# Optimization experiments

Measured on AMD Instinct MI355X. Metric: run time of the kernel, lower is better.

Reference implementation:

```python
import jax, jax.numpy as jnp
import numpy as np

N_ATOMS = 100000
N_FEAT = 256
N_MOL = 1024
SCALE = 5.992277830325989
SHIFT = -406274.63784969115


def setup_inputs() -> dict:
    key = jax.random.key(0)
    ks = jax.random.split(key, 8)
    atom_node = jax.random.normal(ks[0], (N_ATOMS, N_FEAT), dtype=jnp.float32)
    batch = jnp.sort(jax.random.randint(ks[1], (N_ATOMS,), 0, N_MOL, dtype=jnp.int64))
    s = 1.0 / np.sqrt(N_FEAT)
    W1 = jax.random.normal(ks[2], (N_FEAT, N_FEAT), dtype=jnp.float32) * s
    b1 = jnp.zeros((N_FEAT,), dtype=jnp.float32)
    W2 = jax.random.normal(ks[3], (N_FEAT, N_FEAT), dtype=jnp.float32) * s
    b2 = jnp.zeros((N_FEAT,), dtype=jnp.float32)
    W3 = jax.random.normal(ks[4], (N_FEAT, 1), dtype=jnp.float32) * s
    b3 = jnp.zeros((1,), dtype=jnp.float32)
    return {"atom_node": atom_node, "batch": batch, "W1": W1, "b1": b1,
            "W2": W2, "b2": b2, "W3": W3, "b3": b3}


def reference(atom_node, batch, W1, b1, W2, b2, W3, b3):
    # atom-wise 3-layer MLP: F -> F -> F -> 1 with SiLU activations
    h = jax.nn.silu(atom_node @ W1 + b1)          # [N, F]
    h = jax.nn.silu(h @ W2 + b2)                  # [N, F]
    e_atom = (h @ W3 + b3)[:, 0]                  # [N]
    # scatter-sum pooling over molecules
    e_mol = jax.ops.segment_sum(e_atom, batch, num_segments=N_MOL)  # [N_MOL]
    # affine rescale (hardcoded scaler constants from the module)
    return e_mol * SCALE + SHIFT
```

## Files before the change

### kernel.cpp

```cpp
#include <hip/hip_runtime.h>
#include <hip/hip_bf16.h>
#include <cstdint>

#define N_ATOMS 100000
#define NFEAT   256
#define NMOL    1024
#define NU      6256

static constexpr float SCALE_C = 5.992277830325989f;
static constexpr float SHIFT_C = -406274.63784969115f;

typedef __attribute__((ext_vector_type(8))) short short8;
typedef __attribute__((ext_vector_type(4))) float float4_t;

__device__ __forceinline__ unsigned short f2bf(float x) {
    union { float f; uint32_t u; } v; v.f = x;
    uint32_t r = (v.u + 0x7fffu + ((v.u >> 16) & 1u)) >> 16;
    return (unsigned short)r;
}

__device__ __forceinline__ uint32_t pk(float lo, float hi) {
    union { float f; uint32_t u; } a, b; a.f = lo; b.f = hi;
    return __builtin_amdgcn_perm(b.u + 0x8000u, a.u + 0x8000u, 0x07060302u);
}

__device__ __forceinline__ float silu(float x) {
    return x / (1.0f + __expf(-x));
}

__device__ __forceinline__ void async16(void* lds, const void* g) {
    __builtin_amdgcn_global_load_lds(
        (const __attribute__((address_space(1))) unsigned int*)(uintptr_t)g,
        (__attribute__((address_space(3))) unsigned int*)(uint32_t)(uintptr_t)lds,
        16, 0, 0);
}

__device__ __forceinline__ short8 wfrag(const unsigned short* Wlds, int n, int kc) {
    return *(const short8*)&Wlds[((kc >> 4) << 15) + n * 128 +
                                 ((((kc & 15) ^ (n & 15)) & 15) << 3)];
}

__global__ void prep(const float* __restrict__ W1, const float* __restrict__ W2,
                     unsigned short* __restrict__ W1i, unsigned short* __restrict__ W2i,
                     float* __restrict__ out) {
    int g = blockIdx.x * 256 + threadIdx.x;
    const float* W = (g < 65536) ? W1 : W2;
    unsigned short* Wi = (g < 65536) ? W1i : W2i;
    int idx = g & 65535;
    int k = idx >> 8, n = idx & 255;
    int kc = (k >> 3) & 15;
    int pos = ((k >> 7) << 15) + n * 128 + (((kc ^ (n & 15)) & 15) << 3) + (k & 7);
    Wi[pos] = f2bf(W[idx]);
    if (g < NMOL) out[g] = SHIFT_C;
}

__global__ __launch_bounds__(512, 2)
void gemm1(const float* __restrict__ A, const unsigned short* __restrict__ Wimg,
           const float* __restrict__ b1, unsigned short* __restrict__ H1) {
    __shared__ unsigned short Wlds[65536];
    __shared__ float b1L[256];
    __shared__ int uctr;

    const int tid = threadIdx.x;
    const int w = tid >> 6, lane = tid & 63;
    const int fl = lane & 15, qd = lane >> 4;

#pragma unroll
    for (int i = 0; i < 16; ++i)
        async16(&Wlds[(w * 16 + i) * 512], Wimg + (w * 16 + i) * 512 + lane * 8);
    if (tid < 64) ((float4*)b1L)[tid] = ((const float4*)b1)[tid];
    if (tid == 0) uctr = 0;
    __syncthreads();

    for (;;) {
        int t = 0;
        if (lane == 0) t = atomicAdd(&uctr, 1);
        t = __shfl(t, 0);
        const int u = blockIdx.x + (t << 8);
        if (u >= NU) break;

        const int row = u * 16 + fl;
        const bool valid = row < N_ATOMS;
        const float* ap = A + (size_t)row * 256 + qd * 8;

        float4 c0, c1;
        if (valid) { c0 = *(const float4*)ap; c1 = *(const float4*)(ap + 4); }
        else       { c0 = make_float4(0, 0, 0, 0); c1 = c0; }

        float4_t acc[16] = {};
#pragma unroll
        for (int s = 0; s < 8; ++s) {
            float4 n0 = make_float4(0, 0, 0, 0), n1 = n0;
            if (s < 7 && valid) {
                n0 = *(const float4*)(ap + (s + 1) * 32);
                n1 = *(const float4*)(ap + (s + 1) * 32 + 4);
            }
            union { uint32_t u4[4]; short8 s8; } cv;
            cv.u4[0] = pk(c0.x, c0.y); cv.u4[1] = pk(c0.z, c0.w);
            cv.u4[2] = pk(c1.x, c1.y); cv.u4[3] = pk(c1.z, c1.w);
            const int kc = s * 4 + qd;
#pragma unroll
            for (int j = 0; j < 16; ++j) {
                short8 wf = wfrag(Wlds, j * 16 + fl, kc);
                acc[j] = __builtin_amdgcn_mfma_f32_16x16x32_bf16(wf, cv.s8, acc[j], 0, 0, 0);
            }
            c0 = n0; c1 = n1;
        }

        if (valid) {
#pragma unroll
            for (int j = 0; j < 16; ++j) {
                int nb = j * 16 + qd * 4;
                float4 b4 = *(const float4*)&b1L[nb];
                uint2 o;
                o.x = pk(silu(acc[j][0] + b4.x), silu(acc[j][1] + b4.y));
                o.y = pk(silu(acc[j][2] + b4.z), silu(acc[j][3] + b4.w));
                *(uint2*)&H1[(size_t)row * 256 + nb] = o;
            }
        }
    }
}

__global__ __launch_bounds__(512, 2)
void gemm2(const unsigned short* __restrict__ H1, const unsigned short* __restrict__ Wimg,
           const float* __restrict__ b2, const float* __restrict__ W3,
           const float* __restrict__ b3, const int* __restrict__ batch,
           float* __restrict__ out) {
    __shared__ unsigned short Wlds[65536];
    __shared__ float bucket[NMOL];
    __shared__ int uctr;

    const int tid = threadIdx.x;
    const int w = tid >> 6, lane = tid & 63;
    const int fl = lane & 15, qd = lane >> 4;

#pragma unroll
    for (int i = 0; i < 16; ++i)
        async16(&Wlds[(w * 16 + i) * 512], Wimg + (w * 16 + i) * 512 + lane * 8);
    bucket[tid] = 0.0f;
    bucket[tid + 512] = 0.0f;
    if (tid == 0) uctr = 0;
    __syncthreads();

    const float b3v = b3[0];
    float bbv[16], w3v[16];
#pragma unroll
    for (int nt = 0; nt < 16; ++nt) {
        bbv[nt] = b2[nt * 16 + fl];
        w3v[nt] = W3[nt * 16 + fl];
    }

    for (;;) {
        int t = 0;
        if (lane == 0) t = atomicAdd(&uctr, 1);
        t = __shfl(t, 0);
        const int u = blockIdx.x + (t << 8);
        if (u >= NU) break;

        const int ubase = u * 16;
        const int row = ubase + fl;
        const bool valid = row < N_ATOMS;
        const unsigned short* hp = H1 + (size_t)row * 256 + qd * 8;

        short8 h0 = (short8){0, 0, 0, 0, 0, 0, 0, 0};
        if (valid) h0 = *(const short8*)hp;

        float4_t acc[16] = {};
#pragma unroll
        for (int s = 0; s < 8; ++s) {
            short8 hn = (short8){0, 0, 0, 0, 0, 0, 0, 0};
            if (s < 7 && valid) hn = *(const short8*)(hp + (s + 1) * 32);
            const int kc = s * 4 + qd;
#pragma unroll
            for (int nt = 0; nt < 16; ++nt) {
                short8 wf = wfrag(Wlds, nt * 16 + fl, kc);
                acc[nt] = __builtin_amdgcn_mfma_f32_16x16x32_bf16(h0, wf, acc[nt], 0, 0, 0);
            }
            h0 = hn;
        }

        float rs[4] = {};
#pragma unroll
        for (int nt = 0; nt < 16; ++nt)
#pragma unroll
            for (int r = 0; r < 4; ++r)
                rs[r] += silu(acc[nt][r] + bbv[nt]) * w3v[nt];
#pragma unroll
        for (int r = 0; r < 4; ++r) {
            float v = rs[r];
            v += __shfl_xor(v, 1);
            v += __shfl_xor(v, 2);
            v += __shfl_xor(v, 4);
            v += __shfl_xor(v, 8);
            rs[r] = v;
        }
        if (fl == 0) {
            int atom0 = ubase + qd * 4;
            if (atom0 < N_ATOMS) {
                int4 mb = *(const int4*)&batch[atom0];
                float v0 = rs[0] + b3v, v1 = rs[1] + b3v,
                      v2 = rs[2] + b3v, v3 = rs[3] + b3v;
                if (mb.x == mb.w) {
                    atomicAdd(&bucket[mb.x], (v0 + v1) + (v2 + v3));
                } else {
                    atomicAdd(&bucket[mb.x], v0);
                    atomicAdd(&bucket[mb.y], v1);
                    atomicAdd(&bucket[mb.z], v2);
                    atomicAdd(&bucket[mb.w], v3);
                }
            }
        }
    }
    __syncthreads();
#pragma unroll
    for (int i = 0; i < 2; ++i) {
        int m = tid + i * 512;
        float v = bucket[m];
        if (v != 0.0f) atomicAdd(&out[m], v * SCALE_C);
    }
}

extern "C" void kernel_launch(void* const* d_in, const int* in_sizes, int n_in,
                              void* d_out, int out_size, void* d_ws, size_t ws_size,
                              hipStream_t stream) {
    const float* A     = (const float*)d_in[0];
    const int*   batch = (const int*)d_in[1];
    const float* W1    = (const float*)d_in[2];
    const float* b1    = (const float*)d_in[3];
    const float* W2    = (const float*)d_in[4];
    const float* b2    = (const float*)d_in[5];
    const float* W3    = (const float*)d_in[6];
    const float* b3    = (const float*)d_in[7];
    float* out = (float*)d_out;

    unsigned short* H1  = (unsigned short*)d_ws;
    unsigned short* W1i = H1 + (size_t)100096 * NFEAT;
    unsigned short* W2i = W1i + 65536;

    prep<<<dim3(512), 256, 0, stream>>>(W1, W2, W1i, W2i, out);
    gemm1<<<dim3(256), 512, 0, stream>>>(A, W1i, b1, H1);
    gemm2<<<dim3(256), 512, 0, stream>>>(H1, W2i, b2, W3, b3, batch, out);
}
```

Measured before the change: 208.5 us.

## Split output features across two block groups to halve LDS weight footprint

Each GEMM kernel now launches twice as many blocks. Each block loads only half of the weight matrix (128 output columns) into LDS and computes that half of the outputs. LDS per block is halved, so more blocks can be resident per CU (launch bounds raised to 4), which should improve latency hiding. In exchange, every block group re-reads the full input rows (A in fp32 for gemm1, H1 for gemm2), roughly doubling global input traffic, and gemm2 issues twice the bucket atomics.

```diff
diff --git a/kernel.cpp b/kernel.cpp
--- a/kernel.cpp
+++ b/kernel.cpp
@@ -35,9 +35,9 @@
         16, 0, 0);
 }
 
-__device__ __forceinline__ short8 wfrag(const unsigned short* Wlds, int n, int kc) {
-    return *(const short8*)&Wlds[((kc >> 4) << 15) + n * 128 +
-                                 ((((kc & 15) ^ (n & 15)) & 15) << 3)];
+__device__ __forceinline__ short8 wfrag_h(const unsigned short* Wlds, int nl, int kc) {
+    return *(const short8*)&Wlds[((kc >> 4) << 14) + nl * 128 +
+                                 ((((kc & 15) ^ (nl & 15)) & 15) << 3)];
 }
 
 __global__ void prep(const float* __restrict__ W1, const float* __restrict__ W2,
@@ -54,21 +54,26 @@
     if (g < NMOL) out[g] = SHIFT_C;
 }
 
-__global__ __launch_bounds__(512, 2)
+__global__ __launch_bounds__(512, 4)
 void gemm1(const float* __restrict__ A, const unsigned short* __restrict__ Wimg,
            const float* __restrict__ b1, unsigned short* __restrict__ H1) {
-    __shared__ unsigned short Wlds[65536];
-    __shared__ float b1L[256];
+    __shared__ unsigned short Wlds[32768];
+    __shared__ float b1L[128];
     __shared__ int uctr;
 
     const int tid = threadIdx.x;
     const int w = tid >> 6, lane = tid & 63;
     const int fl = lane & 15, qd = lane >> 4;
-
-#pragma unroll
-    for (int i = 0; i < 16; ++i)
-        async16(&Wlds[(w * 16 + i) * 512], Wimg + (w * 16 + i) * 512 + lane * 8);
-    if (tid < 64) ((float4*)b1L)[tid] = ((const float4*)b1)[tid];
+    const int ch = blockIdx.x >> 8;
+    const int bslot = blockIdx.x & 255;
+
+#pragma unroll
+    for (int i = 0; i < 8; ++i) {
+        int c = w * 8 + i;
+        async16(&Wlds[c * 512],
+                Wimg + ((c >> 5) << 15) + (ch << 14) + ((c & 31) << 9) + lane * 8);
+    }
+    if (tid < 32) ((float4*)b1L)[tid] = ((const float4*)(b1 + ch * 128))[tid];
     if (tid == 0) uctr = 0;
     __syncthreads();
 
@@ -76,7 +81,7 @@
         int t = 0;
         if (lane == 0) t = atomicAdd(&uctr, 1);
         t = __shfl(t, 0);
-        const int u = blockIdx.x + (t << 8);
+        const int u = bslot + (t << 8);
         if (u >= NU) break;
 
         const int row = u * 16 + fl;
@@ -87,7 +92,7 @@
         if (valid) { c0 = *(const float4*)ap; c1 = *(const float4*)(ap + 4); }
         else       { c0 = make_float4(0, 0, 0, 0); c1 = c0; }
 
-        float4_t acc[16] = {};
+        float4_t acc[8] = {};
 #pragma unroll
         for (int s = 0; s < 8; ++s) {
             float4 n0 = make_float4(0, 0, 0, 0), n1 = n0;
@@ -100,8 +105,8 @@
             cv.u4[2] = pk(c1.x, c1.y); cv.u4[3] = pk(c1.z, c1.w);
             const int kc = s * 4 + qd;
 #pragma unroll
-            for (int j = 0; j < 16; ++j) {
-                short8 wf = wfrag(Wlds, j * 16 + fl, kc);
+            for (int j = 0; j < 8; ++j) {
+                short8 wf = wfrag_h(Wlds, j * 16 + fl, kc);
                 acc[j] = __builtin_amdgcn_mfma_f32_16x16x32_bf16(wf, cv.s8, acc[j], 0, 0, 0);
             }
             c0 = n0; c1 = n1;
@@ -109,52 +114,57 @@
 
         if (valid) {
 #pragma unroll
-            for (int j = 0; j < 16; ++j) {
-                int nb = j * 16 + qd * 4;
-                float4 b4 = *(const float4*)&b1L[nb];
+            for (int j = 0; j < 8; ++j) {
+                int nl = j * 16 + qd * 4;
+                float4 b4 = *(const float4*)&b1L[nl];
                 uint2 o;
                 o.x = pk(silu(acc[j][0] + b4.x), silu(acc[j][1] + b4.y));
                 o.y = pk(silu(acc[j][2] + b4.z), silu(acc[j][3] + b4.w));
-                *(uint2*)&H1[(size_t)row * 256 + nb] = o;
-            }
-        }
-    }
-}
-
-__global__ __launch_bounds__(512, 2)
+                *(uint2*)&H1[(size_t)row * 256 + ch * 128 + nl] = o;
+            }
+        }
+    }
+}
+
+__global__ __launch_bounds__(512, 4)
 void gemm2(const unsigned short* __restrict__ H1, const unsigned short* __restrict__ Wimg,
            const float* __restrict__ b2, const float* __restrict__ W3,
            const float* __restrict__ b3, const int* __restrict__ batch,
            float* __restrict__ out) {
-    __shared__ unsigned short Wlds[65536];
+    __shared__ unsigned short Wlds[32768];
     __shared__ float bucket[NMOL];
     __shared__ int uctr;
 
     const int tid = threadIdx.x;
     const int w = tid >> 6, lane = tid & 63;
     const int fl = lane & 15, qd = lane >> 4;
-
-#pragma unroll
-    for (int i = 0; i < 16; ++i)
-        async16(&Wlds[(w * 16 + i) * 512], Wimg + (w * 16 + i) * 512 + lane * 8);
+    const int ch = blockIdx.x >> 8;
+    const int bslot = blockIdx.x & 255;
+
+#pragma unroll
+    for (int i = 0; i < 8; ++i) {
+        int c = w * 8 + i;
+        async16(&Wlds[c * 512],
+                Wimg + ((c >> 5) << 15) + (ch << 14) + ((c & 31) << 9) + lane * 8);
+    }
     bucket[tid] = 0.0f;
     bucket[tid + 512] = 0.0f;
     if (tid == 0) uctr = 0;
     __syncthreads();
 
-    const float b3v = b3[0];
-    float bbv[16], w3v[16];
-#pragma unroll
-    for (int nt = 0; nt < 16; ++nt) {
-        bbv[nt] = b2[nt * 16 + fl];
-        w3v[nt] = W3[nt * 16 + fl];
+    const float b3v = (ch == 0) ? b3[0] : 0.0f;
+    float bbv[8], w3v[8];
+#pragma unroll
+    for (int nt = 0; nt < 8; ++nt) {
+        bbv[nt] = b2[ch * 128 + nt * 16 + fl];
+        w3v[nt] = W3[ch * 128 + nt * 16 + fl];
     }
 
     for (;;) {
         int t = 0;
         if (lane == 0) t = atomicAdd(&uctr, 1);
         t = __shfl(t, 0);
-        const int u = blockIdx.x + (t << 8);
+        const int u = bslot + (t << 8);
         if (u >= NU) break;
 
         const int ubase = u * 16;
@@ -165,15 +175,15 @@
         short8 h0 = (short8){0, 0, 0, 0, 0, 0, 0, 0};
         if (valid) h0 = *(const short8*)hp;
 
-        float4_t acc[16] = {};
+        float4_t acc[8] = {};
 #pragma unroll
         for (int s = 0; s < 8; ++s) {
             short8 hn = (short8){0, 0, 0, 0, 0, 0, 0, 0};
             if (s < 7 && valid) hn = *(const short8*)(hp + (s + 1) * 32);
             const int kc = s * 4 + qd;
 #pragma unroll
-            for (int nt = 0; nt < 16; ++nt) {
-                short8 wf = wfrag(Wlds, nt * 16 + fl, kc);
+            for (int nt = 0; nt < 8; ++nt) {
+                short8 wf = wfrag_h(Wlds, nt * 16 + fl, kc);
                 acc[nt] = __builtin_amdgcn_mfma_f32_16x16x32_bf16(h0, wf, acc[nt], 0, 0, 0);
             }
             h0 = hn;
@@ -181,7 +191,7 @@
 
         float rs[4] = {};
 #pragma unroll
-        for (int nt = 0; nt < 16; ++nt)
+        for (int nt = 0; nt < 8; ++nt)
 #pragma unroll
             for (int r = 0; r < 4; ++r)
                 rs[r] += silu(acc[nt][r] + bbv[nt]) * w3v[nt];
@@ -238,6 +248,6 @@
     unsigned short* W2i = W1i + 65536;
 
     prep<<<dim3(512), 256, 0, stream>>>(W1, W2, W1i, W2i, out);
-    gemm1<<<dim3(256), 512, 0, stream>>>(A, W1i, b1, H1);
-    gemm2<<<dim3(256), 512, 0, stream>>>(H1, W2i, b2, W3, b3, batch, out);
-}
+    gemm1<<<dim3(512), 512, 0, stream>>>(A, W1i, b1, H1);
+    gemm2<<<dim3(512), 512, 0, stream>>>(H1, W2i, b2, W3, b3, batch, out);
+}
```

Measured after the change: 210.8 us. Within noise of the previous version (+1.1%).

## Pre-convert activations to bf16 in prep and prefetch full row tiles

Applied to the files above, without the earlier changes.

The prep kernel now also converts the fp32 atom features to a padded bf16 buffer, zero-filling the pad rows. gemm1 therefore reads half the bytes per tile and no longer needs row-validity checks. Both GEMMs load all eight K-slices of a row tile up front and fetch the next work index early, and gemm2 moves b2/W3 from registers into LDS. The extra pass over A adds a full read plus a bf16 write before gemm1, and the up-front loads raise register pressure.

```diff
diff --git a/kernel.cpp b/kernel.cpp
--- a/kernel.cpp
+++ b/kernel.cpp
@@ -6,6 +6,7 @@
 #define NFEAT   256
 #define NMOL    1024
 #define NU      6256
+#define NPAD    100096
 
 static constexpr float SCALE_C = 5.992277830325989f;
 static constexpr float SHIFT_C = -406274.63784969115f;
@@ -41,21 +42,40 @@
 }
 
 __global__ void prep(const float* __restrict__ W1, const float* __restrict__ W2,
+                     const float* __restrict__ A,
                      unsigned short* __restrict__ W1i, unsigned short* __restrict__ W2i,
-                     float* __restrict__ out) {
-    int g = blockIdx.x * 256 + threadIdx.x;
-    const float* W = (g < 65536) ? W1 : W2;
-    unsigned short* Wi = (g < 65536) ? W1i : W2i;
-    int idx = g & 65535;
-    int k = idx >> 8, n = idx & 255;
-    int kc = (k >> 3) & 15;
-    int pos = ((k >> 7) << 15) + n * 128 + (((kc ^ (n & 15)) & 15) << 3) + (k & 7);
-    Wi[pos] = f2bf(W[idx]);
-    if (g < NMOL) out[g] = SHIFT_C;
+                     unsigned short* __restrict__ Ab, float* __restrict__ out) {
+    const int b = blockIdx.x, tid = threadIdx.x;
+    if (b < 512) {
+        int g = b * 256 + tid;
+        const float* W = (g < 65536) ? W1 : W2;
+        unsigned short* Wi = (g < 65536) ? W1i : W2i;
+        int idx = g & 65535;
+        int k = idx >> 8, n = idx & 255;
+        int kc = (k >> 3) & 15;
+        int pos = ((k >> 7) << 15) + n * 128 + (((kc ^ (n & 15)) & 15) << 3) + (k & 7);
+        Wi[pos] = f2bf(W[idx]);
+        if (g < NMOL) out[g] = SHIFT_C;
+    } else if (b < 6762) {
+        int t = (b - 512) * 256 + tid;
+        const float4* af = (const float4*)(A + (size_t)t * 16);
+        float4 x0 = af[0], x1 = af[1], x2 = af[2], x3 = af[3];
+        uint4 o0 = make_uint4(pk(x0.x, x0.y), pk(x0.z, x0.w),
+                              pk(x1.x, x1.y), pk(x1.z, x1.w));
+        uint4 o1 = make_uint4(pk(x2.x, x2.y), pk(x2.z, x2.w),
+                              pk(x3.x, x3.y), pk(x3.z, x3.w));
+        ((uint4*)Ab)[(size_t)t * 2]     = o0;
+        ((uint4*)Ab)[(size_t)t * 2 + 1] = o1;
+    } else {
+        int idx = (b - 6762) * 256 + tid;
+        uint4 z = make_uint4(0, 0, 0, 0);
+        ((uint4*)(Ab + (size_t)N_ATOMS * 256))[idx * 2]     = z;
+        ((uint4*)(Ab + (size_t)N_ATOMS * 256))[idx * 2 + 1] = z;
+    }
 }
 
 __global__ __launch_bounds__(512, 2)
-void gemm1(const float* __restrict__ A, const unsigned short* __restrict__ Wimg,
+void gemm1(const unsigned short* __restrict__ Ab, const unsigned short* __restrict__ Wimg,
            const float* __restrict__ b1, unsigned short* __restrict__ H1) {
     __shared__ unsigned short Wlds[65536];
     __shared__ float b1L[256];
@@ -64,6 +84,7 @@
     const int tid = threadIdx.x;
     const int w = tid >> 6, lane = tid & 63;
     const int fl = lane & 15, qd = lane >> 4;
+    const int bslot = blockIdx.x;
 
 #pragma unroll
     for (int i = 0; i < 16; ++i)
@@ -72,51 +93,41 @@
     if (tid == 0) uctr = 0;
     __syncthreads();
 
+    int t;
+    { int tt = 0; if (lane == 0) tt = atomicAdd(&uctr, 1); t = __shfl(tt, 0); }
+
     for (;;) {
-        int t = 0;
-        if (lane == 0) t = atomicAdd(&uctr, 1);
-        t = __shfl(t, 0);
-        const int u = blockIdx.x + (t << 8);
+        const int u = bslot + (t << 8);
         if (u >= NU) break;
 
         const int row = u * 16 + fl;
-        const bool valid = row < N_ATOMS;
-        const float* ap = A + (size_t)row * 256 + qd * 8;
-
-        float4 c0, c1;
-        if (valid) { c0 = *(const float4*)ap; c1 = *(const float4*)(ap + 4); }
-        else       { c0 = make_float4(0, 0, 0, 0); c1 = c0; }
+        const unsigned short* ap = Ab + (size_t)row * 256 + qd * 8;
+
+        short8 a[8];
+#pragma unroll
+        for (int s = 0; s < 8; ++s) a[s] = *(const short8*)(ap + s * 32);
+
+        { int tt = 0; if (lane == 0) tt = atomicAdd(&uctr, 1); t = __shfl(tt, 0); }
 
         float4_t acc[16] = {};
 #pragma unroll
         for (int s = 0; s < 8; ++s) {
-            float4 n0 = make_float4(0, 0, 0, 0), n1 = n0;
-            if (s < 7 && valid) {
-                n0 = *(const float4*)(ap + (s + 1) * 32);
-                n1 = *(const float4*)(ap + (s + 1) * 32 + 4);
-            }
-            union { uint32_t u4[4]; short8 s8; } cv;
-            cv.u4[0] = pk(c0.x, c0.y); cv.u4[1] = pk(c0.z, c0.w);
-            cv.u4[2] = pk(c1.x, c1.y); cv.u4[3] = pk(c1.z, c1.w);
             const int kc = s * 4 + qd;
 #pragma unroll
             for (int j = 0; j < 16; ++j) {
                 short8 wf = wfrag(Wlds, j * 16 + fl, kc);
-                acc[j] = __builtin_amdgcn_mfma_f32_16x16x32_bf16(wf, cv.s8, acc[j], 0, 0, 0);
+                acc[j] = __builtin_amdgcn_mfma_f32_16x16x32_bf16(wf, a[s], acc[j], 0, 0, 0);
             }
-            c0 = n0; c1 = n1;
-        }
-
-        if (valid) {
-#pragma unroll
-            for (int j = 0; j < 16; ++j) {
-                int nb = j * 16 + qd * 4;
-                float4 b4 = *(const float4*)&b1L[nb];
-                uint2 o;
-                o.x = pk(silu(acc[j][0] + b4.x), silu(acc[j][1] + b4.y));
-                o.y = pk(silu(acc[j][2] + b4.z), silu(acc[j][3] + b4.w));
-                *(uint2*)&H1[(size_t)row * 256 + nb] = o;
-            }
+        }
+
+#pragma unroll
+        for (int j = 0; j < 16; ++j) {
+            int nb = j * 16 + qd * 4;
+            float4 b4 = *(const float4*)&b1L[nb];
+            uint2 o;
+            o.x = pk(silu(acc[j][0] + b4.x), silu(acc[j][1] + b4.y));
+            o.y = pk(silu(acc[j][2] + b4.z), silu(acc[j][3] + b4.w));
+            *(uint2*)&H1[(size_t)row * 256 + nb] = o;
         }
     }
 }
@@ -128,63 +139,65 @@
            float* __restrict__ out) {
     __shared__ unsigned short Wlds[65536];
     __shared__ float bucket[NMOL];
+    __shared__ float bL2[256], w3L[256];
     __shared__ int uctr;
 
     const int tid = threadIdx.x;
     const int w = tid >> 6, lane = tid & 63;
     const int fl = lane & 15, qd = lane >> 4;
+    const int bslot = blockIdx.x;
 
 #pragma unroll
     for (int i = 0; i < 16; ++i)
         async16(&Wlds[(w * 16 + i) * 512], Wimg + (w * 16 + i) * 512 + lane * 8);
     bucket[tid] = 0.0f;
     bucket[tid + 512] = 0.0f;
+    if (tid < 256) {
+        bL2[tid] = b2[tid];
+        w3L[tid] = W3[tid];
+    }
     if (tid == 0) uctr = 0;
     __syncthreads();
 
     const float b3v = b3[0];
-    float bbv[16], w3v[16];
-#pragma unroll
-    for (int nt = 0; nt < 16; ++nt) {
-        bbv[nt] = b2[nt * 16 + fl];
-        w3v[nt] = W3[nt * 16 + fl];
-    }
+
+    int t;
+    { int tt = 0; if (lane == 0) tt = atomicAdd(&uctr, 1); t = __shfl(tt, 0); }
 
     for (;;) {
-        int t = 0;
-        if (lane == 0) t = atomicAdd(&uctr, 1);
-        t = __shfl(t, 0);
-        const int u = blockIdx.x + (t << 8);
+        const int u = bslot + (t << 8);
         if (u >= NU) break;
 
         const int ubase = u * 16;
         const int row = ubase + fl;
-        const bool valid = row < N_ATOMS;
         const unsigned short* hp = H1 + (size_t)row * 256 + qd * 8;
 
-        short8 h0 = (short8){0, 0, 0, 0, 0, 0, 0, 0};
-        if (valid) h0 = *(const short8*)hp;
+        short8 h[8];
+#pragma unroll
+        for (int s = 0; s < 8; ++s) h[s] = *(const short8*)(hp + s * 32);
+
+        { int tt = 0; if (lane == 0) tt = atomicAdd(&uctr, 1); t = __shfl(tt, 0); }
 
         float4_t acc[16] = {};
 #pragma unroll
         for (int s = 0; s < 8; ++s) {
-            short8 hn = (short8){0, 0, 0, 0, 0, 0, 0, 0};
-            if (s < 7 && valid) hn = *(const short8*)(hp + (s + 1) * 32);
             const int kc = s * 4 + qd;
 #pragma unroll
             for (int nt = 0; nt < 16; ++nt) {
                 short8 wf = wfrag(Wlds, nt * 16 + fl, kc);
-                acc[nt] = __builtin_amdgcn_mfma_f32_16x16x32_bf16(h0, wf, acc[nt], 0, 0, 0);
+                acc[nt] = __builtin_amdgcn_mfma_f32_16x16x32_bf16(h[s], wf, acc[nt], 0, 0, 0);
             }
-            h0 = hn;
         }
 
         float rs[4] = {};
 #pragma unroll
-        for (int nt = 0; nt < 16; ++nt)
+        for (int nt = 0; nt < 16; ++nt) {
+            float bb = bL2[nt * 16 + fl];
+            float w3 = w3L[nt * 16 + fl];
 #pragma unroll
             for (int r = 0; r < 4; ++r)
-                rs[r] += silu(acc[nt][r] + bbv[nt]) * w3v[nt];
+                rs[r] += silu(acc[nt][r] + bb) * w3;
+        }
 #pragma unroll
         for (int r = 0; r < 4; ++r) {
             float v = rs[r];
@@ -234,10 +247,11 @@
     float* out = (float*)d_out;
 
     unsigned short* H1  = (unsigned short*)d_ws;
-    unsigned short* W1i = H1 + (size_t)100096 * NFEAT;
+    unsigned short* W1i = H1 + (size_t)NPAD * NFEAT;
     unsigned short* W2i = W1i + 65536;
-
-    prep<<<dim3(512), 256, 0, stream>>>(W1, W2, W1i, W2i, out);
-    gemm1<<<dim3(256), 512, 0, stream>>>(A, W1i, b1, H1);
+    unsigned short* Ab  = W2i + 65536;
+
+    prep<<<dim3(6768), 256, 0, stream>>>(W1, W2, A, W1i, W2i, Ab, out);
+    gemm1<<<dim3(256), 512, 0, stream>>>(Ab, W1i, b1, H1);
     gemm2<<<dim3(256), 512, 0, stream>>>(H1, W2i, b2, W3, b3, batch, out);
 }
```

Result: slower. 613.0 us (+193.9%).
